# Kernel tuning notes

Measured on AMD Instinct MI355X. Metric: run time of the kernel, lower is better.

## Reference

```python
import jax, jax.numpy as jnp
import numpy as np

B, S, D, H = 2, 2048, 512, 8
HD = D // H
SPARSITY = 0.15
KTOP = max(1, int(S * SPARSITY))          # 307 important rows
HALF_WIN = min(32, S // 4) // 2           # 16 -> window |i-j| <= 16
RC = min(16, S // 8)                      # 16 random links per query token


def setup_inputs() -> dict:
    key = jax.random.key(0)
    ks = jax.random.split(key, 8)
    s = 0.02
    return {
        "x":  jax.random.normal(ks[0], (B, S, D), jnp.float32),
        "Wq": jax.random.normal(ks[1], (D, D), jnp.float32) * s,
        "bq": jnp.zeros((D,), jnp.float32),
        "Wk": jax.random.normal(ks[2], (D, D), jnp.float32) * s,
        "bk": jnp.zeros((D,), jnp.float32),
        "Wv": jax.random.normal(ks[3], (D, D), jnp.float32) * s,
        "bv": jnp.zeros((D,), jnp.float32),
        "Wo": jax.random.normal(ks[4], (D, D), jnp.float32) * s,
        "bo": jnp.zeros((D,), jnp.float32),
        "Ws1": jax.random.normal(ks[5], (D, D // 2), jnp.float32) * s,
        "bs1": jnp.zeros((D // 2,), jnp.float32),
        "Ws2": jax.random.normal(ks[6], (D // 2, 1), jnp.float32) * s,
        "bs2": jnp.zeros((1,), jnp.float32),
        # models torch.randperm(S)[:RC] per (b, i); duplicates are harmless for set-to-1
        "rand_idx": jax.random.randint(ks[7], (B, S, RC), 0, S, jnp.int32),
    }


def _sparse_mask(x, Ws1, bs1, Ws2, bs2, rand_idx):
    # importance scorer: Linear -> ReLU -> Linear -> Sigmoid, squeeze(-1)
    imp = jax.nn.sigmoid(jax.nn.relu(x @ Ws1 + bs1) @ Ws2 + bs2)[..., 0]  # [B,S]
    _, top_idx = jax.lax.top_k(imp, KTOP)                                  # [B,KTOP]
    brange = jnp.arange(B)
    row_imp = jnp.zeros((B, S), bool).at[brange[:, None], top_idx].set(True)
    idx = jnp.arange(S)
    win = jnp.abs(idx[:, None] - idx[None, :]) <= HALF_WIN                 # [S,S]
    rmask = jnp.zeros((B, S, S), bool).at[
        brange[:, None, None], idx[None, :, None], rand_idx].set(True)    # [B,S,S]
    mask = row_imp[:, :, None] | win[None, :, :] | rmask                   # [B,S,S]
    tril = idx[:, None] >= idx[None, :]                                    # causal (mask * (causal==0))
    return mask & tril


def reference(x, Wq, bq, Wk, bk, Wv, bv, Wo, bo, Ws1, bs1, Ws2, bs2, rand_idx):
    allowed = _sparse_mask(x, Ws1, bs1, Ws2, bs2, rand_idx)                # [B,S,S] bool
    q = (x @ Wq + bq).reshape(B, S, H, HD).transpose(0, 2, 1, 3)           # [B,H,S,HD]
    k = (x @ Wk + bk).reshape(B, S, H, HD).transpose(0, 2, 1, 3)
    v = (x @ Wv + bv).reshape(B, S, H, HD).transpose(0, 2, 1, 3)
    scores = jnp.einsum('bhid,bhjd->bhij', q, k) / jnp.sqrt(jnp.float32(HD))
    scores = jnp.where(allowed[:, None, :, :], scores, -jnp.inf)
    attn = jax.nn.softmax(scores, axis=-1)                                 # every row has j=i allowed
    out = jnp.einsum('bhij,bhjd->bhid', attn, v)
    out = out.transpose(0, 2, 1, 3).reshape(B, S, D)
    return out @ Wo + bo
```

## Files before the change

### kernel.cpp

```cpp
#include <hip/hip_runtime.h>
#include <math.h>

typedef unsigned short u16;
typedef unsigned int u32;
typedef unsigned long long u64;
typedef short bf16x8 __attribute__((ext_vector_type(8)));
typedef float f32x4 __attribute__((ext_vector_type(4)));

constexpr int NB = 2, NS = 2048, ND = 512, NH = 8, NHD = 64;
constexpr int NKTOP = 307, NHWIN = 16, NRC = 16;
constexpr int NILIST = 320;
constexpr int NCHUNK = 4;
constexpr int NKMAX = 33;
constexpr int LDSPAD = 40;

__device__ __forceinline__ u16 f2bf(float f) {
  u32 u = __builtin_bit_cast(u32, f);
  u32 r = (u + 0x7FFFu + ((u >> 16) & 1u)) >> 16;
  return (u16)r;
}
__device__ __forceinline__ float bf2f(short v) {
  return __builtin_bit_cast(float, (u32)(u16)v << 16);
}

__global__ __launch_bounds__(256) void csa_cvt_w(const float* __restrict__ W0, const float* __restrict__ W1,
                                                 const float* __restrict__ W2, const float* __restrict__ W3,
                                                 u16* __restrict__ wt) {
  __shared__ float tile[32][33];
  int w = blockIdx.z;
  const float* src = (w == 0) ? W0 : (w == 1) ? W1 : (w == 2) ? W2 : W3;
  int kb = blockIdx.x * 32, nb = blockIdx.y * 32;
  int tx = threadIdx.x & 31, ty = threadIdx.x >> 5;
  for (int i = ty; i < 32; i += 8) tile[i][tx] = src[(size_t)(kb + i) * ND + nb + tx];
  __syncthreads();
  u16* dst = wt + (size_t)w * ND * ND;
  for (int i = ty; i < 32; i += 8) dst[(size_t)(nb + i) * ND + kb + tx] = f2bf(tile[tx][i]);
}

__global__ __launch_bounds__(256) void csa_scorer(const float* __restrict__ x, const float* __restrict__ Ws1,
                                                  const float* __restrict__ bs1, const float* __restrict__ Ws2,
                                                  float* __restrict__ logit) {
  __shared__ float As[32][33];
  __shared__ float Bs[32][68];
  const int tid = threadIdx.x;
  const int m0 = blockIdx.x * 32, n0 = blockIdx.y * 64;
  const int r2 = (tid >> 4) * 2;
  const int c4 = (tid & 15) * 4;
  float acc[2][4] = {};
  const int arow = tid & 31, aks = (tid >> 5) * 4;
  const int bk = tid >> 3, bc = (tid & 7) * 8;
  for (int k0 = 0; k0 < ND; k0 += 32) {
    __syncthreads();
    float4 av = *(const float4*)(&x[(size_t)(m0 + arow) * ND + k0 + aks]);
    As[aks + 0][arow] = av.x;
    As[aks + 1][arow] = av.y;
    As[aks + 2][arow] = av.z;
    As[aks + 3][arow] = av.w;
    *(float4*)(&Bs[bk][bc]) = *(const float4*)(&Ws1[(size_t)(k0 + bk) * 256 + n0 + bc]);
    *(float4*)(&Bs[bk][bc + 4]) = *(const float4*)(&Ws1[(size_t)(k0 + bk) * 256 + n0 + bc + 4]);
    __syncthreads();
    for (int k = 0; k < 32; k++) {
      float a0 = As[k][r2], a1 = As[k][r2 + 1];
      float4 b = *(const float4*)(&Bs[k][c4]);
      acc[0][0] += a0 * b.x; acc[0][1] += a0 * b.y; acc[0][2] += a0 * b.z; acc[0][3] += a0 * b.w;
      acc[1][0] += a1 * b.x; acc[1][1] += a1 * b.y; acc[1][2] += a1 * b.z; acc[1][3] += a1 * b.w;
    }
  }
  float4 w2 = *(const float4*)(&Ws2[n0 + c4]);
  float4 b1 = *(const float4*)(&bs1[n0 + c4]);
  float p0 = fmaxf(acc[0][0] + b1.x, 0.f) * w2.x + fmaxf(acc[0][1] + b1.y, 0.f) * w2.y +
             fmaxf(acc[0][2] + b1.z, 0.f) * w2.z + fmaxf(acc[0][3] + b1.w, 0.f) * w2.w;
  float p1 = fmaxf(acc[1][0] + b1.x, 0.f) * w2.x + fmaxf(acc[1][1] + b1.y, 0.f) * w2.y +
             fmaxf(acc[1][2] + b1.z, 0.f) * w2.z + fmaxf(acc[1][3] + b1.w, 0.f) * w2.w;
  for (int off = 1; off < 16; off <<= 1) {
    p0 += __shfl_xor(p0, off, 64);
    p1 += __shfl_xor(p1, off, 64);
  }
  if ((tid & 15) == 0) {
    atomicAdd(&logit[m0 + r2], p0);
    atomicAdd(&logit[m0 + r2 + 1], p1);
  }
}

__global__ __launch_bounds__(256) void csa_rank(const float* __restrict__ imp, int* __restrict__ rowimp) {
  __shared__ float vals[NS];
  const int b = blockIdx.y;
  {
    int t8 = threadIdx.x * 8;
    *(float4*)(&vals[t8]) = *(const float4*)(&imp[b * NS + t8]);
    *(float4*)(&vals[t8 + 4]) = *(const float4*)(&imp[b * NS + t8 + 4]);
  }
  __syncthreads();
  const int wave = threadIdx.x >> 6, lane = threadIdx.x & 63;
  const int s0 = blockIdx.x * 8 + wave * 2;
  const int s1 = s0 + 1;
  const float v0 = vals[s0], v1 = vals[s1];
  int r0 = 0, r1 = 0;
  for (int t = lane; t < NS; t += 64) {
    float u = vals[t];
    r0 += (int)((u > v0) | ((u == v0) & (t < s0)));
    r1 += (int)((u > v1) | ((u == v1) & (t < s1)));
  }
  for (int off = 1; off < 64; off <<= 1) {
    r0 += __shfl_xor(r0, off, 64);
    r1 += __shfl_xor(r1, off, 64);
  }
  if (lane == 0) {
    rowimp[b * NS + s0] = (r0 < NKTOP) ? 1 : 0;
    rowimp[b * NS + s1] = (r1 < NKTOP) ? 1 : 0;
  }
}

__global__ __launch_bounds__(256) void csa_ilist(const int* __restrict__ rowimp, int* __restrict__ ilist) {
  __shared__ int cs[256];
  int b = blockIdx.x, t = threadIdx.x;
  int flags[8], sum = 0;
  for (int k = 0; k < 8; k++) {
    flags[k] = rowimp[b * NS + t * 8 + k];
    sum += flags[k];
  }
  cs[t] = sum;
  __syncthreads();
  for (int off = 1; off < 256; off <<= 1) {
    int v = (t >= off) ? cs[t - off] : 0;
    __syncthreads();
    cs[t] += v;
    __syncthreads();
  }
  int pos = cs[t] - sum;
  for (int k = 0; k < 8; k++)
    if (flags[k]) ilist[b * NILIST + pos++] = t * 8 + k;
  if (t < NILIST - NKTOP) ilist[b * NILIST + NKTOP + t] = -1;
}

__global__ __launch_bounds__(256) void csa_gemm_qkv(const float* __restrict__ x, const u16* __restrict__ Bt,
                                                    const float* __restrict__ bq, const float* __restrict__ bk,
                                                    const float* __restrict__ bv, u16* __restrict__ qb,
                                                    u16* __restrict__ kb, u16* __restrict__ vtb,
                                                    u16* __restrict__ vb) {
  __shared__ __attribute__((aligned(16))) u16 As[128 * LDSPAD];
  __shared__ __attribute__((aligned(16))) u16 Bs[64 * LDSPAD];
  const int tid = threadIdx.x;
  const int wave = tid >> 6, lane = tid & 63;
  const int quad = lane >> 4, col = lane & 15;
  const int m0 = blockIdx.x * 128;
  const int n0 = blockIdx.y * 64;
  const f32x4 zf = {0.f, 0.f, 0.f, 0.f};
  f32x4 acc[2][4] = {{zf, zf, zf, zf}, {zf, zf, zf, zf}};
  const int sar = tid >> 1, sak = (tid & 1) * 16;
  const int sbr = tid >> 2, sbk = (tid & 3) * 8;
  for (int k0 = 0; k0 < ND; k0 += 32) {
    __syncthreads();
    {
      const float* xp = &x[(size_t)(m0 + sar) * ND + k0 + sak];
      float4 v0 = *(const float4*)(xp), v1 = *(const float4*)(xp + 4);
      float4 v2 = *(const float4*)(xp + 8), v3 = *(const float4*)(xp + 12);
      u32 w0 = (u32)f2bf(v0.x) | ((u32)f2bf(v0.y) << 16);
      u32 w1 = (u32)f2bf(v0.z) | ((u32)f2bf(v0.w) << 16);
      u32 w2 = (u32)f2bf(v1.x) | ((u32)f2bf(v1.y) << 16);
      u32 w3 = (u32)f2bf(v1.z) | ((u32)f2bf(v1.w) << 16);
      u32 w4 = (u32)f2bf(v2.x) | ((u32)f2bf(v2.y) << 16);
      u32 w5 = (u32)f2bf(v2.z) | ((u32)f2bf(v2.w) << 16);
      u32 w6 = (u32)f2bf(v3.x) | ((u32)f2bf(v3.y) << 16);
      u32 w7 = (u32)f2bf(v3.z) | ((u32)f2bf(v3.w) << 16);
      u32* ap = (u32*)&As[sar * LDSPAD + sak];
      ap[0] = w0; ap[1] = w1; ap[2] = w2; ap[3] = w3;
      ap[4] = w4; ap[5] = w5; ap[6] = w6; ap[7] = w7;
    }
    *(uint4*)(&Bs[sbr * LDSPAD + sbk]) = *(const uint4*)(&Bt[(size_t)(n0 + sbr) * ND + k0 + sbk]);
    __syncthreads();
    bf16x8 af0 = *(const bf16x8*)(&As[(wave * 32 + col) * LDSPAD + quad * 8]);
    bf16x8 af1 = *(const bf16x8*)(&As[(wave * 32 + 16 + col) * LDSPAD + quad * 8]);
    for (int c = 0; c < 4; c++) {
      bf16x8 bfr = *(const bf16x8*)(&Bs[(c * 16 + col) * LDSPAD + quad * 8]);
      acc[0][c] = __builtin_amdgcn_mfma_f32_16x16x32_bf16(af0, bfr, acc[0][c], 0, 0, 0);
      acc[1][c] = __builtin_amdgcn_mfma_f32_16x16x32_bf16(af1, bfr, acc[1][c], 0, 0, 0);
    }
  }
  const int w = n0 >> 9;
  const float* bias = (w == 0) ? bq : (w == 1) ? bk : bv;
  for (int c = 0; c < 4; c++) {
    const int ng = n0 + c * 16 + col;
    const int nn = ng & 511, hh = nn >> 6, hd = nn & 63;
    const float bvv = bias[nn];
    for (int r = 0; r < 2; r++) {
      for (int rr = 0; rr < 4; rr++) {
        const int m = m0 + wave * 32 + r * 16 + quad * 4 + rr;
        const int bb = m >> 11, s = m & (NS - 1);
        u16 v16 = f2bf(acc[r][c][rr] + bvv);
        if (w == 0) qb[((size_t)(bb * NH + hh) * NS + s) * NHD + hd] = v16;
        else if (w == 1) kb[((size_t)(bb * NH + hh) * NS + s) * NHD + hd] = v16;
        else {
          vtb[((size_t)(bb * NH + hh) * NHD + hd) * NS + s] = v16;
          vb[((size_t)(bb * NH + hh) * NS + s) * NHD + hd] = v16;
        }
      }
    }
  }
}

__global__ __launch_bounds__(256) void csa_gemm_out(const u16* __restrict__ A, const u16* __restrict__ Bt,
                                                    const float* __restrict__ bias, float* __restrict__ outp) {
  __shared__ __attribute__((aligned(16))) u16 As[64 * LDSPAD];
  __shared__ __attribute__((aligned(16))) u16 Bs[64 * LDSPAD];
  const int tid = threadIdx.x;
  const int wave = tid >> 6, lane = tid & 63;
  const int quad = lane >> 4, col = lane & 15;
  const int m0 = blockIdx.x * 64;
  const int n0 = blockIdx.y * 64;
  const f32x4 zf = {0.f, 0.f, 0.f, 0.f};
  f32x4 acc[4] = {zf, zf, zf, zf};
  const int lrow = tid >> 2, lk = (tid & 3) * 8;
  for (int k0 = 0; k0 < ND; k0 += 32) {
    __syncthreads();
    *(uint4*)(&As[lrow * LDSPAD + lk]) = *(const uint4*)(&A[(size_t)(m0 + lrow) * ND + k0 + lk]);
    *(uint4*)(&Bs[lrow * LDSPAD + lk]) = *(const uint4*)(&Bt[(size_t)(n0 + lrow) * ND + k0 + lk]);
    __syncthreads();
    bf16x8 af = *(const bf16x8*)(&As[(wave * 16 + col) * LDSPAD + quad * 8]);
    for (int nt = 0; nt < 4; nt++) {
      bf16x8 bfr = *(const bf16x8*)(&Bs[(nt * 16 + col) * LDSPAD + quad * 8]);
      acc[nt] = __builtin_amdgcn_mfma_f32_16x16x32_bf16(af, bfr, acc[nt], 0, 0, 0);
    }
  }
  for (int nt = 0; nt < 4; nt++) {
    const int n = n0 + nt * 16 + col;
    const float bvv = bias[n];
    for (int r = 0; r < 4; r++) {
      const int m = m0 + wave * 16 + quad * 4 + r;
      outp[(size_t)m * ND + n] = acc[nt][r] + bvv;
    }
  }
}

__global__ __launch_bounds__(64) void csa_attn_imp(const u16* __restrict__ qb, const u16* __restrict__ kb,
                                                   const u16* __restrict__ vtb, const int* __restrict__ ilist,
                                                   float* __restrict__ pbuf) {
  const int lane = threadIdx.x;
  const int quad = lane >> 4, col = lane & 15;
  const int qt = blockIdx.x;
  const int chunk = blockIdx.y;
  const int bh = blockIdx.z;
  const int b = bh >> 3, h = bh & 7;

  const int* il = ilist + b * NILIST;
  const u16* qptr = qb + (size_t)(b * NH + h) * NS * NHD;
  const u16* kptr = kb + (size_t)(b * NH + h) * NS * NHD;
  const u16* vptr = vtb + (size_t)(b * NH + h) * NHD * NS;

  const int iq = il[qt * 16 + col];
  const int qrow = (iq < 0) ? 0 : iq;
  bf16x8 qf0 = *(const bf16x8*)(qptr + qrow * NHD + quad * 8);
  bf16x8 qf1 = *(const bf16x8*)(qptr + qrow * NHD + 32 + quad * 8);

  const f32x4 zf = {0.f, 0.f, 0.f, 0.f};
  float m_r[4], l_r[4];
  f32x4 of[4];
  int irow[4];
  for (int r = 0; r < 4; r++) {
    m_r[r] = -INFINITY;
    l_r[r] = 0.f;
    irow[r] = il[qt * 16 + quad * 4 + r];
  }
  for (int n = 0; n < 4; n++) of[n] = zf;

  __shared__ __attribute__((aligned(16))) u16 Pl[16 * LDSPAD];

  const int max_i = il[(qt * 16 + 15 > NKTOP - 1) ? (NKTOP - 1) : (qt * 16 + 15)];
  const int ntiles = (max_i >> 5) + 1;
  for (int t = chunk; t < ntiles; t += NCHUNK) {
    const int j0 = t * 32;
    f32x4 c0 = zf, c1 = zf;
    {
      bf16x8 k00 = *(const bf16x8*)(kptr + (j0 + col) * NHD + quad * 8);
      bf16x8 k01 = *(const bf16x8*)(kptr + (j0 + col) * NHD + 32 + quad * 8);
      c0 = __builtin_amdgcn_mfma_f32_16x16x32_bf16(qf0, k00, c0, 0, 0, 0);
      c0 = __builtin_amdgcn_mfma_f32_16x16x32_bf16(qf1, k01, c0, 0, 0, 0);
      bf16x8 k10 = *(const bf16x8*)(kptr + (j0 + 16 + col) * NHD + quad * 8);
      bf16x8 k11 = *(const bf16x8*)(kptr + (j0 + 16 + col) * NHD + 32 + quad * 8);
      c1 = __builtin_amdgcn_mfma_f32_16x16x32_bf16(qf0, k10, c1, 0, 0, 0);
      c1 = __builtin_amdgcn_mfma_f32_16x16x32_bf16(qf1, k11, c1, 0, 0, 0);
    }
    const int j_0 = j0 + col, j_1 = j0 + 16 + col;
    float p0s[4], p1s[4], alpha[4];
    for (int r = 0; r < 4; r++) {
      const int i = irow[r];
      float s0 = (j_0 <= i) ? c0[r] * 0.125f : -INFINITY;
      float s1 = (j_1 <= i) ? c1[r] * 0.125f : -INFINITY;
      float vmax = fmaxf(s0, s1);
      for (int off = 1; off < 16; off <<= 1) vmax = fmaxf(vmax, __shfl_xor(vmax, off, 64));
      float newm = fmaxf(m_r[r], vmax);
      bool dead = (newm == -INFINITY);
      float a = dead ? 1.f : __expf(m_r[r] - newm);
      float p0 = dead ? 0.f : __expf(s0 - newm);
      float p1 = dead ? 0.f : __expf(s1 - newm);
      float psum = p0 + p1;
      for (int off = 1; off < 16; off <<= 1) psum += __shfl_xor(psum, off, 64);
      m_r[r] = newm;
      l_r[r] = l_r[r] * a + psum;
      alpha[r] = a;
      p0s[r] = p0;
      p1s[r] = p1;
    }
    for (int n = 0; n < 4; n++)
      for (int r = 0; r < 4; r++) of[n][r] *= alpha[r];
    __syncthreads();
    for (int r = 0; r < 4; r++) {
      Pl[(quad * 4 + r) * LDSPAD + col] = f2bf(p0s[r]);
      Pl[(quad * 4 + r) * LDSPAD + 16 + col] = f2bf(p1s[r]);
    }
    __syncthreads();
    bf16x8 pf = *(const bf16x8*)(&Pl[col * LDSPAD + quad * 8]);
    for (int vn = 0; vn < 4; vn++) {
      bf16x8 vf = *(const bf16x8*)(vptr + (size_t)(vn * 16 + col) * NS + j0 + quad * 8);
      of[vn] = __builtin_amdgcn_mfma_f32_16x16x32_bf16(pf, vf, of[vn], 0, 0, 0);
    }
  }
  float* pr = pbuf + ((size_t)(bh * NCHUNK + chunk) * NILIST + qt * 16) * 66;
  for (int r = 0; r < 4; r++) {
    const int row = quad * 4 + r;
    if (col == 0) {
      pr[row * 66 + 0] = m_r[r];
      pr[row * 66 + 1] = l_r[r];
    }
    for (int vn = 0; vn < 4; vn++)
      pr[row * 66 + 2 + vn * 16 + col] = of[vn][r];
  }
}

__global__ __launch_bounds__(64) void csa_merge(const float* __restrict__ pbuf, const int* __restrict__ ilist,
                                                u16* __restrict__ attnb) {
  const int kp = blockIdx.x, h = blockIdx.y, b = blockIdx.z;
  const int lane = threadIdx.x;
  const int z = b * NH + h;
  float mc[NCHUNK], lc[NCHUNK], mstar = -INFINITY;
  for (int c = 0; c < NCHUNK; c++) {
    const float* base = pbuf + ((size_t)(z * NCHUNK + c) * NILIST + kp) * 66;
    mc[c] = base[0];
    lc[c] = base[1];
    mstar = fmaxf(mstar, mc[c]);
  }
  float lsum = 0.f, osum = 0.f;
  for (int c = 0; c < NCHUNK; c++) {
    const float* base = pbuf + ((size_t)(z * NCHUNK + c) * NILIST + kp) * 66;
    float w = (mc[c] == -INFINITY) ? 0.f : __expf(mc[c] - mstar);
    lsum += w * lc[c];
    osum += w * base[2 + lane];
  }
  const int i = ilist[b * NILIST + kp];
  attnb[((size_t)(b * NS + i) * NH + h) * NHD + lane] = f2bf(osum / lsum);
}

__global__ __launch_bounds__(256) void csa_attn_sparse(const u16* __restrict__ qb, const u16* __restrict__ kb,
                                                       const u16* __restrict__ vb, const int* __restrict__ rowimp,
                                                       const int* __restrict__ rand_idx, u16* __restrict__ attnb) {
  __shared__ __attribute__((aligned(16))) u16 ql[4][64];
  __shared__ float pl[4][64];
  __shared__ int jl[4][64];
  const int wave = threadIdx.x >> 6, lane = threadIdx.x & 63;
  const int i = blockIdx.x * 4 + wave;
  const int h = blockIdx.y, b = blockIdx.z;
  const int imp = rowimp[b * NS + i];

  const u16* qrow = qb + ((size_t)(b * NH + h) * NS + i) * NHD;
  const u16* kbase = kb + (size_t)(b * NH + h) * NS * NHD;
  const u16* vbase = vb + (size_t)(b * NH + h) * NS * NHD;

  if (lane < 8) *(bf16x8*)(&ql[wave][lane * 8]) = *(const bf16x8*)(qrow + lane * 8);
  __syncthreads();

  int j = 0, valid = 0;
  if (lane < 17) {
    j = i - NHWIN + lane;
    valid = (j >= 0);
  } else if (lane < 17 + NRC) {
    const int* rr = rand_idx + ((size_t)b * NS + i) * NRC;
    int c = lane - 17;
    j = rr[c];
    valid = (j <= i - NHWIN - 1);
    for (int cp = 0; cp < c; cp++) valid &= (rr[cp] != j);
  }
  const int jr = valid ? j : 0;

  float s = 0.f;
  const u16* krow = kbase + (size_t)jr * NHD;
  for (int c8 = 0; c8 < 8; c8++) {
    bf16x8 kv = *(const bf16x8*)(krow + c8 * 8);
    bf16x8 qv = *(const bf16x8*)(&ql[wave][c8 * 8]);
    for (int e = 0; e < 8; e++) s += bf2f(qv[e]) * bf2f(kv[e]);
  }
  s = valid ? s * 0.125f : -INFINITY;

  float vmax = s;
  for (int off = 1; off < 64; off <<= 1) vmax = fmaxf(vmax, __shfl_xor(vmax, off, 64));
  float p = valid ? __expf(s - vmax) : 0.f;
  float lsum = p;
  for (int off = 1; off < 64; off <<= 1) lsum += __shfl_xor(lsum, off, 64);

  pl[wave][lane] = p;
  jl[wave][lane] = jr;
  __syncthreads();

  float o = 0.f;
  for (int jj = 0; jj < NKMAX; jj++) {
    float pj = pl[wave][jj];
    int jk = jl[wave][jj];
    o += pj * bf2f((short)vbase[(size_t)jk * NHD + lane]);
  }
  if (!imp)
    attnb[((size_t)(b * NS + i) * NH + h) * NHD + lane] = f2bf(o / lsum);
}

extern "C" void kernel_launch(void* const* d_in, const int* in_sizes, int n_in,
                              void* d_out, int out_size, void* d_ws, size_t ws_size,
                              hipStream_t stream) {
  const float* x = (const float*)d_in[0];
  const float* bq = (const float*)d_in[2];
  const float* bk = (const float*)d_in[4];
  const float* bv = (const float*)d_in[6];
  const float* bo = (const float*)d_in[8];
  const float* Ws1 = (const float*)d_in[9];
  const float* bs1 = (const float*)d_in[10];
  const float* Ws2 = (const float*)d_in[11];
  const int* rand_idx = (const int*)d_in[13];
  float* out = (float*)d_out;

  char* p = (char*)d_ws;
  u16* wt = (u16*)p;         p += (size_t)4 * ND * ND * 2;
  u16* qbuf = (u16*)p;       p += (size_t)NB * NH * NS * NHD * 2;
  u16* kbuf = (u16*)p;       p += (size_t)NB * NH * NS * NHD * 2;
  u16* vtbuf = (u16*)p;      p += (size_t)NB * NH * NHD * NS * 2;
  u16* vbuf = (u16*)p;       p += (size_t)NB * NH * NS * NHD * 2;
  u16* attnb = (u16*)p;      p += (size_t)NB * NS * ND * 2;
  float* logit = (float*)p;  p += (size_t)NB * NS * 4;
  int* rowimp = (int*)p;     p += (size_t)NB * NS * 4;
  int* ilist = (int*)p;      p += (size_t)NB * NILIST * 4;
  float* pbuf = (float*)p;

  csa_cvt_w<<<dim3(16, 16, 4), 256, 0, stream>>>((const float*)d_in[1], (const float*)d_in[3],
                                                 (const float*)d_in[5], (const float*)d_in[7], wt);

  (void)hipMemsetAsync(logit, 0, (size_t)NB * NS * 4, stream);
  csa_scorer<<<dim3(NB * NS / 32, 4), 256, 0, stream>>>(x, Ws1, bs1, Ws2, logit);
  csa_rank<<<dim3(NS / 8, NB), 256, 0, stream>>>(logit, rowimp);
  csa_ilist<<<dim3(NB), 256, 0, stream>>>(rowimp, ilist);

  csa_gemm_qkv<<<dim3(32, 24), 256, 0, stream>>>(x, wt, bq, bk, bv, qbuf, kbuf, vtbuf, vbuf);

  csa_attn_imp<<<dim3(NILIST / 16, NCHUNK, NB * NH), 64, 0, stream>>>(qbuf, kbuf, vtbuf, ilist, pbuf);
  csa_attn_sparse<<<dim3(NS / 4, NH, NB), 256, 0, stream>>>(qbuf, kbuf, vbuf, rowimp, rand_idx, attnb);
  csa_merge<<<dim3(NKTOP, NH, NB), 64, 0, stream>>>(pbuf, ilist, attnb);

  csa_gemm_out<<<dim3(64, 8), 256, 0, stream>>>(attnb, wt + 3 * (size_t)ND * ND, bo, out);
}
```

Baseline: 220.4 us.

## Compact non-important rows for sparse attention and drop scorer atomics

```diff
diff --git a/kernel.cpp b/kernel.cpp
--- a/kernel.cpp
+++ b/kernel.cpp
@@ -10,8 +10,9 @@
 constexpr int NB = 2, NS = 2048, ND = 512, NH = 8, NHD = 64;
 constexpr int NKTOP = 307, NHWIN = 16, NRC = 16;
 constexpr int NILIST = 320;
+constexpr int NSPAR = NS - NKTOP;
+constexpr int NSPAD = 1744;
 constexpr int NCHUNK = 4;
-constexpr int NKMAX = 33;
 constexpr int LDSPAD = 40;
 
 __device__ __forceinline__ u16 f2bf(float f) {
@@ -39,7 +40,7 @@
 
 __global__ __launch_bounds__(256) void csa_scorer(const float* __restrict__ x, const float* __restrict__ Ws1,
                                                   const float* __restrict__ bs1, const float* __restrict__ Ws2,
-                                                  float* __restrict__ logit) {
+                                                  float* __restrict__ part) {
   __shared__ float As[32][33];
   __shared__ float Bs[32][68];
   const int tid = threadIdx.x;
@@ -77,18 +78,20 @@
     p1 += __shfl_xor(p1, off, 64);
   }
   if ((tid & 15) == 0) {
-    atomicAdd(&logit[m0 + r2], p0);
-    atomicAdd(&logit[m0 + r2 + 1], p1);
-  }
-}
-
-__global__ __launch_bounds__(256) void csa_rank(const float* __restrict__ imp, int* __restrict__ rowimp) {
+    part[(size_t)(m0 + r2) * 4 + blockIdx.y] = p0;
+    part[(size_t)(m0 + r2 + 1) * 4 + blockIdx.y] = p1;
+  }
+}
+
+__global__ __launch_bounds__(256) void csa_rank(const float* __restrict__ part, int* __restrict__ rowimp) {
   __shared__ float vals[NS];
   const int b = blockIdx.y;
   {
     int t8 = threadIdx.x * 8;
-    *(float4*)(&vals[t8]) = *(const float4*)(&imp[b * NS + t8]);
-    *(float4*)(&vals[t8 + 4]) = *(const float4*)(&imp[b * NS + t8 + 4]);
+    for (int e = 0; e < 8; e++) {
+      float4 pp = *(const float4*)(&part[(size_t)(b * NS + t8 + e) * 4]);
+      vals[t8 + e] = (pp.x + pp.y) + (pp.z + pp.w);
+    }
   }
   __syncthreads();
   const int wave = threadIdx.x >> 6, lane = threadIdx.x & 63;
@@ -111,7 +114,8 @@
   }
 }
 
-__global__ __launch_bounds__(256) void csa_ilist(const int* __restrict__ rowimp, int* __restrict__ ilist) {
+__global__ __launch_bounds__(256) void csa_ilist(const int* __restrict__ rowimp, int* __restrict__ ilist,
+                                                 int* __restrict__ nlist) {
   __shared__ int cs[256];
   int b = blockIdx.x, t = threadIdx.x;
   int flags[8], sum = 0;
@@ -128,9 +132,13 @@
     __syncthreads();
   }
   int pos = cs[t] - sum;
-  for (int k = 0; k < 8; k++)
-    if (flags[k]) ilist[b * NILIST + pos++] = t * 8 + k;
+  for (int k = 0; k < 8; k++) {
+    int r = t * 8 + k;
+    if (flags[k]) ilist[b * NILIST + pos++] = r;
+    else nlist[b * NSPAD + (r - pos)] = r;
+  }
   if (t < NILIST - NKTOP) ilist[b * NILIST + NKTOP + t] = -1;
+  if (t < NSPAD - NSPAR) nlist[b * NSPAD + NSPAR + t] = -1;
 }
 
 __global__ __launch_bounds__(256) void csa_gemm_qkv(const float* __restrict__ x, const u16* __restrict__ Bt,
@@ -351,62 +359,79 @@
 }
 
 __global__ __launch_bounds__(256) void csa_attn_sparse(const u16* __restrict__ qb, const u16* __restrict__ kb,
-                                                       const u16* __restrict__ vb, const int* __restrict__ rowimp,
+                                                       const u16* __restrict__ vb, const int* __restrict__ nlist,
                                                        const int* __restrict__ rand_idx, u16* __restrict__ attnb) {
   __shared__ __attribute__((aligned(16))) u16 ql[4][64];
-  __shared__ float pl[4][64];
-  __shared__ int jl[4][64];
+  __shared__ float pl[4][33];
+  __shared__ int jl[4][33];
   const int wave = threadIdx.x >> 6, lane = threadIdx.x & 63;
-  const int i = blockIdx.x * 4 + wave;
+  const int slot = blockIdx.x * 4 + wave;
   const int h = blockIdx.y, b = blockIdx.z;
-  const int imp = rowimp[b * NS + i];
-
-  const u16* qrow = qb + ((size_t)(b * NH + h) * NS + i) * NHD;
+  const int i = nlist[b * NSPAD + slot];
+  const int iv = (i < 0) ? 0 : i;
+
+  const u16* qrow = qb + ((size_t)(b * NH + h) * NS + iv) * NHD;
   const u16* kbase = kb + (size_t)(b * NH + h) * NS * NHD;
   const u16* vbase = vb + (size_t)(b * NH + h) * NS * NHD;
 
   if (lane < 8) *(bf16x8*)(&ql[wave][lane * 8]) = *(const bf16x8*)(qrow + lane * 8);
   __syncthreads();
 
-  int j = 0, valid = 0;
-  if (lane < 17) {
-    j = i - NHWIN + lane;
+  float sd = bf2f((short)ql[wave][lane]) * bf2f((short)kbase[(size_t)iv * NHD + lane]);
+  for (int off = 1; off < 64; off <<= 1) sd += __shfl_xor(sd, off, 64);
+  sd *= 0.125f;
+
+  const int c = lane >> 1, half = lane & 1;
+  int j, valid;
+  if (c < 16) {
+    j = i - NHWIN + c;
     valid = (j >= 0);
-  } else if (lane < 17 + NRC) {
-    const int* rr = rand_idx + ((size_t)b * NS + i) * NRC;
-    int c = lane - 17;
-    j = rr[c];
+  } else {
+    const int* rr = rand_idx + ((size_t)b * NS + iv) * NRC;
+    const int cr = c - 16;
+    j = rr[cr];
     valid = (j <= i - NHWIN - 1);
-    for (int cp = 0; cp < c; cp++) valid &= (rr[cp] != j);
+    for (int cp = 0; cp < cr; cp++) valid &= (rr[cp] != j);
   }
   const int jr = valid ? j : 0;
-
   float s = 0.f;
-  const u16* krow = kbase + (size_t)jr * NHD;
-  for (int c8 = 0; c8 < 8; c8++) {
-    bf16x8 kv = *(const bf16x8*)(krow + c8 * 8);
-    bf16x8 qv = *(const bf16x8*)(&ql[wave][c8 * 8]);
-    for (int e = 0; e < 8; e++) s += bf2f(qv[e]) * bf2f(kv[e]);
-  }
+  {
+    const u16* krow = kbase + (size_t)jr * NHD + half * 32;
+    for (int c8 = 0; c8 < 4; c8++) {
+      bf16x8 kv = *(const bf16x8*)(krow + c8 * 8);
+      bf16x8 qv = *(const bf16x8*)(&ql[wave][half * 32 + c8 * 8]);
+      for (int e = 0; e < 8; e++) s += bf2f(qv[e]) * bf2f(kv[e]);
+    }
+  }
+  s += __shfl_xor(s, 1, 64);
   s = valid ? s * 0.125f : -INFINITY;
 
-  float vmax = s;
-  for (int off = 1; off < 64; off <<= 1) vmax = fmaxf(vmax, __shfl_xor(vmax, off, 64));
-  float p = valid ? __expf(s - vmax) : 0.f;
-  float lsum = p;
-  for (int off = 1; off < 64; off <<= 1) lsum += __shfl_xor(lsum, off, 64);
-
-  pl[wave][lane] = p;
-  jl[wave][lane] = jr;
+  float smax = s;
+  for (int off = 1; off < 64; off <<= 1) smax = fmaxf(smax, __shfl_xor(smax, off, 64));
+  smax = fmaxf(smax, sd);
+  float p = valid ? __expf(s - smax) : 0.f;
+  float pd = __expf(sd - smax);
+  float pm = (half == 0) ? p : 0.f;
+  for (int off = 1; off < 64; off <<= 1) pm += __shfl_xor(pm, off, 64);
+  const float lsum = pm + pd;
+
+  if (half == 0) {
+    pl[wave][c] = p;
+    jl[wave][c] = jr;
+  }
+  if (lane == 0) {
+    pl[wave][32] = pd;
+    jl[wave][32] = iv;
+  }
   __syncthreads();
 
   float o = 0.f;
-  for (int jj = 0; jj < NKMAX; jj++) {
-    float pj = pl[wave][jj];
-    int jk = jl[wave][jj];
+  for (int jj = 0; jj < 33; jj++) {
+    const int jk = __builtin_amdgcn_readfirstlane(jl[wave][jj]);
+    const float pj = pl[wave][jj];
     o += pj * bf2f((short)vbase[(size_t)jk * NHD + lane]);
   }
-  if (!imp)
+  if (i >= 0)
     attnb[((size_t)(b * NS + i) * NH + h) * NHD + lane] = f2bf(o / lsum);
 }
 
@@ -431,23 +456,23 @@
   u16* vtbuf = (u16*)p;      p += (size_t)NB * NH * NHD * NS * 2;
   u16* vbuf = (u16*)p;       p += (size_t)NB * NH * NS * NHD * 2;
   u16* attnb = (u16*)p;      p += (size_t)NB * NS * ND * 2;
-  float* logit = (float*)p;  p += (size_t)NB * NS * 4;
+  float* part = (float*)p;   p += (size_t)NB * NS * 4 * 4;
   int* rowimp = (int*)p;     p += (size_t)NB * NS * 4;
   int* ilist = (int*)p;      p += (size_t)NB * NILIST * 4;
+  int* nlist = (int*)p;      p += (size_t)NB * NSPAD * 4;
   float* pbuf = (float*)p;
 
   csa_cvt_w<<<dim3(16, 16, 4), 256, 0, stream>>>((const float*)d_in[1], (const float*)d_in[3],
                                                  (const float*)d_in[5], (const float*)d_in[7], wt);
 
-  (void)hipMemsetAsync(logit, 0, (size_t)NB * NS * 4, stream);
-  csa_scorer<<<dim3(NB * NS / 32, 4), 256, 0, stream>>>(x, Ws1, bs1, Ws2, logit);
-  csa_rank<<<dim3(NS / 8, NB), 256, 0, stream>>>(logit, rowimp);
-  csa_ilist<<<dim3(NB), 256, 0, stream>>>(rowimp, ilist);
+  csa_scorer<<<dim3(NB * NS / 32, 4), 256, 0, stream>>>(x, Ws1, bs1, Ws2, part);
+  csa_rank<<<dim3(NS / 8, NB), 256, 0, stream>>>(part, rowimp);
+  csa_ilist<<<dim3(NB), 256, 0, stream>>>(rowimp, ilist, nlist);
 
   csa_gemm_qkv<<<dim3(32, 24), 256, 0, stream>>>(x, wt, bq, bk, bv, qbuf, kbuf, vtbuf, vbuf);
 
   csa_attn_imp<<<dim3(NILIST / 16, NCHUNK, NB * NH), 64, 0, stream>>>(qbuf, kbuf, vtbuf, ilist, pbuf);
-  csa_attn_sparse<<<dim3(NS / 4, NH, NB), 256, 0, stream>>>(qbuf, kbuf, vbuf, rowimp, rand_idx, attnb);
+  csa_attn_sparse<<<dim3(NSPAD / 4, NH, NB), 256, 0, stream>>>(qbuf, kbuf, vbuf, nlist, rand_idx, attnb);
   csa_merge<<<dim3(NKTOP, NH, NB), 64, 0, stream>>>(pbuf, ilist, attnb);
 
   csa_gemm_out<<<dim3(64, 8), 256, 0, stream>>>(attnb, wt + 3 * (size_t)ND * ND, bo, out);
```

After: 213.1 us. 1.03x faster.
